# Optimization experiments

Hardware: AMD Instinct MI355X
Metric: run time of the kernel (lower is better)

The kernel has to match this reference:

```python
import jax, jax.numpy as jnp
import numpy as np

V, D, A = 100000, 128, 64
L, N, K = 3, 20000, 16


def setup_inputs() -> dict:
    key = jax.random.key(0)
    k1, k2, k3, k4, k5, k6 = jax.random.split(key, 6)
    Leaf_emb = jax.random.normal(k1, (V, D), dtype=jnp.float32)
    nodes = jax.random.randint(k2, (L, N), 0, V, dtype=jnp.int32)
    neighbors = jax.random.randint(k3, (L, N, K), 0, V, dtype=jnp.int32)
    masks = jnp.zeros((L, N, K), dtype=jnp.float32)  # additive mask, 0 = valid
    weights = jax.random.normal(k4, (L, N, K), dtype=jnp.float32)
    W_att = jax.random.uniform(k5, (2 * D, A), dtype=jnp.float32)
    b_att = jnp.zeros((A,), dtype=jnp.float32)
    v_att = jax.random.uniform(k6, (A,), dtype=jnp.float32)
    return {"Leaf_emb": Leaf_emb, "nodes": nodes, "neighbors": neighbors,
            "masks": masks, "weights": weights,
            "W_att": W_att, "b_att": b_att, "v_att": v_att}


def reference(Leaf_emb, nodes, neighbors, masks, weights, W_att, b_att, v_att):
    # Sequential over L tree levels (fixed, small): each level gathers node and
    # neighbor embeddings, scores neighbors with a 2-layer attention MLP,
    # combines masked-softmax attention with softmax'd structural weights,
    # sums neighbor embeddings and scatters the result back into W_tmp.
    W_tmp = Leaf_emb
    n_levels = nodes.shape[0]
    for i in range(n_levels):
        node = nodes[i]                      # [N] (constant across K in original)
        neighbor = neighbors[i]              # [N, K]
        mask = masks[i]                      # [N, K] additive
        weight = weights[i]                  # [N, K]
        node_tmp = Leaf_emb[node][:, None, :]          # [N, 1, D] from ORIGINAL emb
        neighbor_tmp = W_tmp[neighbor]                 # [N, K, D] from running emb
        node_b = jnp.broadcast_to(node_tmp, neighbor_tmp.shape)
        att_in = jnp.concatenate([node_b, neighbor_tmp], axis=2)  # [N, K, 2D]
        mlp = jax.nn.leaky_relu(att_in @ W_att + b_att, 0.01)     # [N, K, A]
        pre = mlp @ v_att                                         # [N, K]
        att = jax.nn.softmax(pre + mask, axis=1) * jax.nn.softmax(weight, axis=1)
        temp_emb = jnp.einsum('nkd,nk->nd', neighbor_tmp, att)    # [N, D]
        W_tmp = W_tmp.at[node].set(temp_emb)
    return W_tmp
```

## Files before the change

### kernel.cpp

```cpp
#include <hip/hip_runtime.h>
#include <math.h>

#define V 100000
#define D 128
#define A 64
#define LVLS 3
#define NN 20000
#define KK 16
#define BK 32
#define ASTRIDE 34
#define BSTRIDE 68

__global__ __launch_bounds__(256, 2)
void proj_kernel(const float* __restrict__ Wsrc, const float* __restrict__ Wmat,
                 const float* __restrict__ bias, const int* __restrict__ idx,
                 int dst_from_idx, int nrows, float* __restrict__ outp) {
    __shared__ float As[128 * ASTRIDE];
    __shared__ float Bs[BK * BSTRIDE];
    int t = threadIdx.x;
    int tx = t & 15, ty = t >> 4;
    int r0 = blockIdx.x * 128;

    const float* srcp[4];
#pragma unroll
    for (int jj = 0; jj < 4; ++jj) {
        int r = r0 + (t >> 3) + 32 * jj;
        int rr = r < nrows ? r : nrows - 1;
        int s = idx ? idx[rr] : rr;
        srcp[jj] = Wsrc + (size_t)s * D + ((t & 7) << 2);
    }

    float4 bv = make_float4(0.f, 0.f, 0.f, 0.f);
    if (bias) bv = *(const float4*)(bias + 4 * tx);
    float acc[8][4];
#pragma unroll
    for (int i = 0; i < 8; ++i) {
        acc[i][0] = bv.x; acc[i][1] = bv.y; acc[i][2] = bv.z; acc[i][3] = bv.w;
    }

    for (int k0 = 0; k0 < D; k0 += BK) {
#pragma unroll
        for (int jj = 0; jj < 4; ++jj) {
            float4 v = *(const float4*)(srcp[jj] + k0);
            *(float4*)&As[((t >> 3) + 32 * jj) * ASTRIDE + ((t & 7) << 2)] = v;
        }
#pragma unroll
        for (int ss = 0; ss < 2; ++ss) {
            int s = t + 256 * ss;
            int kB = s >> 4, c4 = (s & 15) << 2;
            *(float4*)&Bs[kB * BSTRIDE + c4] =
                *(const float4*)(Wmat + (size_t)(k0 + kB) * A + c4);
        }
        __syncthreads();
#pragma unroll
        for (int kc = 0; kc < BK; kc += 4) {
            float4 b0 = *(const float4*)&Bs[(kc + 0) * BSTRIDE + 4 * tx];
            float4 b1 = *(const float4*)&Bs[(kc + 1) * BSTRIDE + 4 * tx];
            float4 b2 = *(const float4*)&Bs[(kc + 2) * BSTRIDE + 4 * tx];
            float4 b3 = *(const float4*)&Bs[(kc + 3) * BSTRIDE + 4 * tx];
#pragma unroll
            for (int i = 0; i < 8; ++i) {
                float4 a = *(const float4*)&As[(8 * ty + i) * ASTRIDE + kc];
                acc[i][0] = fmaf(a.x, b0.x, acc[i][0]);
                acc[i][0] = fmaf(a.y, b1.x, acc[i][0]);
                acc[i][0] = fmaf(a.z, b2.x, acc[i][0]);
                acc[i][0] = fmaf(a.w, b3.x, acc[i][0]);
                acc[i][1] = fmaf(a.x, b0.y, acc[i][1]);
                acc[i][1] = fmaf(a.y, b1.y, acc[i][1]);
                acc[i][1] = fmaf(a.z, b2.y, acc[i][1]);
                acc[i][1] = fmaf(a.w, b3.y, acc[i][1]);
                acc[i][2] = fmaf(a.x, b0.z, acc[i][2]);
                acc[i][2] = fmaf(a.y, b1.z, acc[i][2]);
                acc[i][2] = fmaf(a.z, b2.z, acc[i][2]);
                acc[i][2] = fmaf(a.w, b3.z, acc[i][2]);
                acc[i][3] = fmaf(a.x, b0.w, acc[i][3]);
                acc[i][3] = fmaf(a.y, b1.w, acc[i][3]);
                acc[i][3] = fmaf(a.z, b2.w, acc[i][3]);
                acc[i][3] = fmaf(a.w, b3.w, acc[i][3]);
            }
        }
        __syncthreads();
    }

#pragma unroll
    for (int i = 0; i < 8; ++i) {
        int gr = r0 + 8 * ty + i;
        if (gr < nrows) {
            int s = idx ? idx[gr] : gr;
            int dst = dst_from_idx ? s : gr;
            float4 o = make_float4(acc[i][0], acc[i][1], acc[i][2], acc[i][3]);
            *(float4*)(outp + (size_t)dst * A + 4 * tx) = o;
        }
    }
}

__global__ __launch_bounds__(256)
void attn_kernel(const float* __restrict__ Wc, const float* __restrict__ proj,
                 const float* __restrict__ nodeproj, const int* __restrict__ neigh,
                 const float* __restrict__ maskp, const float* __restrict__ weightp,
                 const float* __restrict__ v_att, float* __restrict__ tmp) {
    int lane = threadIdx.x & 63;
    int n = blockIdx.x * 4 + (threadIdx.x >> 6);
    int k16 = lane & 15, q = lane >> 4;

    int   nbk = neigh[n * KK + k16];
    float wv  = weightp[n * KK + k16];
    float mk  = maskp[n * KK + k16];

    const float* npr = nodeproj + (size_t)n * A + q * 16;
    const float* var = v_att + q * 16;
    const float* pr  = proj + (size_t)nbk * A + q * 16;

    float part = 0.f;
#pragma unroll
    for (int j = 0; j < 16; j += 4) {
        float4 npv = *(const float4*)(npr + j);
        float4 vav = *(const float4*)(var + j);
        float4 pv  = *(const float4*)(pr + j);
        float x;
        x = npv.x + pv.x; x = fmaxf(x, 0.01f * x); part = fmaf(x, vav.x, part);
        x = npv.y + pv.y; x = fmaxf(x, 0.01f * x); part = fmaf(x, vav.y, part);
        x = npv.z + pv.z; x = fmaxf(x, 0.01f * x); part = fmaf(x, vav.z, part);
        x = npv.w + pv.w; x = fmaxf(x, 0.01f * x); part = fmaf(x, vav.w, part);
    }
    part += __shfl_xor(part, 16);
    part += __shfl_xor(part, 32);
    float pre = part + mk;

    float mp = pre, mw = wv;
#pragma unroll
    for (int off = 8; off >= 1; off >>= 1) {
        mp = fmaxf(mp, __shfl_xor(mp, off));
        mw = fmaxf(mw, __shfl_xor(mw, off));
    }
    float ep = __expf(pre - mp), ew = __expf(wv - mw);
    float sp = ep, sw = ew;
#pragma unroll
    for (int off = 8; off >= 1; off >>= 1) {
        sp += __shfl_xor(sp, off);
        sw += __shfl_xor(sw, off);
    }
    float att = (ep / sp) * (ew / sw);

    float ax = 0.f, ay = 0.f;
#pragma unroll
    for (int k = 0; k < KK; ++k) {
        int nb   = __shfl(nbk, k);
        float ak = __shfl(att, k);
        float2 e = *(const float2*)&Wc[(size_t)nb * D + 2 * lane];
        ax = fmaf(e.x, ak, ax); ay = fmaf(e.y, ak, ay);
    }
    float2 o; o.x = ax; o.y = ay;
    *(float2*)&tmp[(size_t)n * D + 2 * lane] = o;
}

__global__ void amax3_kernel(const int* __restrict__ nodes, int* __restrict__ claims, int total) {
    int i = blockIdx.x * 256 + threadIdx.x;
    if (i < total) {
        int lvl = i / NN, pos = i - lvl * NN;
        atomicMax(&claims[(size_t)lvl * V + nodes[i]], pos);
    }
}

__global__ void scatter_kernel(const int* __restrict__ nodes_l, const int* __restrict__ claim,
                               const float* __restrict__ tmp, float* __restrict__ out, int n) {
    int tid = blockIdx.x * 256 + threadIdx.x;
    int nn = tid >> 7, d = tid & 127;
    if (nn < n) {
        int v = nodes_l[nn];
        if (claim[v] == nn) out[(size_t)v * D + d] = tmp[(size_t)nn * D + d];
    }
}

extern "C" void kernel_launch(void* const* d_in, const int* in_sizes, int n_in,
                              void* d_out, int out_size, void* d_ws, size_t ws_size,
                              hipStream_t stream) {
    const float* Leaf    = (const float*)d_in[0];
    const int*   nodes   = (const int*)d_in[1];
    const int*   neigh   = (const int*)d_in[2];
    const float* masks   = (const float*)d_in[3];
    const float* weights = (const float*)d_in[4];
    const float* Watt    = (const float*)d_in[5];
    const float* batt    = (const float*)d_in[6];
    const float* vatt    = (const float*)d_in[7];
    float* out = (float*)d_out;

    char* ws = (char*)d_ws;
    float* proj     = (float*)ws;
    float* nodeproj = (float*)(ws + (size_t)V * A * 4);
    float* tmp      = (float*)(ws + (size_t)(V * A + LVLS * NN * A) * 4);
    int*   claims   = (int*)(ws + (size_t)(V * A + LVLS * NN * A + NN * D) * 4);

    hipMemcpyAsync(out, Leaf, (size_t)V * D * sizeof(float), hipMemcpyDeviceToDevice, stream);
    hipMemsetAsync(claims, 0xFF, (size_t)LVLS * V * sizeof(int), stream);

    proj_kernel<<<(LVLS * NN + 127) / 128, 256, 0, stream>>>(
        Leaf, Watt, batt, nodes, 0, LVLS * NN, nodeproj);
    proj_kernel<<<(V + 127) / 128, 256, 0, stream>>>(
        out, Watt + D * A, nullptr, nullptr, 0, V, proj);
    amax3_kernel<<<(LVLS * NN + 255) / 256, 256, 0, stream>>>(nodes, claims, LVLS * NN);

    for (int l = 0; l < LVLS; ++l) {
        const int* nodes_l = nodes + l * NN;
        attn_kernel<<<NN / 4, 256, 0, stream>>>(out, proj, nodeproj + (size_t)l * NN * A,
                                                neigh + (size_t)l * NN * KK,
                                                masks + (size_t)l * NN * KK,
                                                weights + (size_t)l * NN * KK, vatt, tmp);
        scatter_kernel<<<(NN * D + 255) / 256, 256, 0, stream>>>(
            nodes_l, claims + (size_t)l * V, tmp, out, NN);
        if (l + 1 < LVLS)
            proj_kernel<<<(NN + 127) / 128, 256, 0, stream>>>(
                out, Watt + D * A, nullptr, nodes_l, 1, NN, proj);
    }
}
```

Measured before the change: 334.5 us.

## Fuse leaf copy into projection, merge scatter with reprojection, widen gather loads

Replaces the separate device copy of Leaf_emb into the output and the two projection launches with one 2D-grid projection kernel. It computes both halves of W_att for all V rows into an interleaved projAll buffer and writes the leaf copy as a side effect. The node-half projection is now indexed by node id instead of being precomputed per level. The per-level scatter and the re-projection kernel are merged into a commit kernel that writes winning rows and their new projections. The attention gather now loads float4 with half-wave splits and a cross-half reduction. This cuts launches and memory passes, at the cost of computing the node projection for all V rows instead of only the 3*N selected ones.

```diff
diff --git a/kernel.cpp b/kernel.cpp
--- a/kernel.cpp
+++ b/kernel.cpp
@@ -10,28 +10,32 @@
 #define BK 32
 #define ASTRIDE 34
 #define BSTRIDE 68
+#define PSTRIDE 128
 
 __global__ __launch_bounds__(256, 2)
-void proj_kernel(const float* __restrict__ Wsrc, const float* __restrict__ Wmat,
-                 const float* __restrict__ bias, const int* __restrict__ idx,
-                 int dst_from_idx, int nrows, float* __restrict__ outp) {
+void projall_kernel(const float* __restrict__ Leaf, const float* __restrict__ Watt,
+                    const float* __restrict__ batt, float* __restrict__ projAll,
+                    float* __restrict__ outp) {
     __shared__ float As[128 * ASTRIDE];
     __shared__ float Bs[BK * BSTRIDE];
     int t = threadIdx.x;
     int tx = t & 15, ty = t >> 4;
     int r0 = blockIdx.x * 128;
+    int half = blockIdx.y;
+    const float* Wmat = Watt + (size_t)half * D * A;
 
     const float* srcp[4];
+    int rg[4];
 #pragma unroll
     for (int jj = 0; jj < 4; ++jj) {
         int r = r0 + (t >> 3) + 32 * jj;
-        int rr = r < nrows ? r : nrows - 1;
-        int s = idx ? idx[rr] : rr;
-        srcp[jj] = Wsrc + (size_t)s * D + ((t & 7) << 2);
+        rg[jj] = r;
+        int rr = r < V ? r : V - 1;
+        srcp[jj] = Leaf + (size_t)rr * D + ((t & 7) << 2);
     }
 
     float4 bv = make_float4(0.f, 0.f, 0.f, 0.f);
-    if (bias) bv = *(const float4*)(bias + 4 * tx);
+    if (half == 0) bv = *(const float4*)(batt + 4 * tx);
     float acc[8][4];
 #pragma unroll
     for (int i = 0; i < 8; ++i) {
@@ -43,6 +47,8 @@
         for (int jj = 0; jj < 4; ++jj) {
             float4 v = *(const float4*)(srcp[jj] + k0);
             *(float4*)&As[((t >> 3) + 32 * jj) * ASTRIDE + ((t & 7) << 2)] = v;
+            if (half == 0 && rg[jj] < V)
+                *(float4*)(outp + (size_t)rg[jj] * D + k0 + ((t & 7) << 2)) = v;
         }
 #pragma unroll
         for (int ss = 0; ss < 2; ++ss) {
@@ -85,31 +91,123 @@
 #pragma unroll
     for (int i = 0; i < 8; ++i) {
         int gr = r0 + 8 * ty + i;
-        if (gr < nrows) {
-            int s = idx ? idx[gr] : gr;
-            int dst = dst_from_idx ? s : gr;
+        if (gr < V) {
             float4 o = make_float4(acc[i][0], acc[i][1], acc[i][2], acc[i][3]);
-            *(float4*)(outp + (size_t)dst * A + 4 * tx) = o;
+            *(float4*)(projAll + (size_t)gr * PSTRIDE + half * 64 + 4 * tx) = o;
+        }
+    }
+}
+
+__global__ __launch_bounds__(256, 2)
+void commit_kernel(const float* __restrict__ tmp, const float* __restrict__ Wmat,
+                   const int* __restrict__ nodes_l, const int* __restrict__ claim,
+                   float* __restrict__ outp, float* __restrict__ projAll, int do_proj) {
+    __shared__ float As[128 * ASTRIDE];
+    __shared__ float Bs[BK * BSTRIDE];
+    int t = threadIdx.x;
+    int tx = t & 15, ty = t >> 4;
+    int r0 = blockIdx.x * 128;
+
+    const float* srcp[4];
+    int vrow[4], win[4];
+#pragma unroll
+    for (int jj = 0; jj < 4; ++jj) {
+        int r = r0 + (t >> 3) + 32 * jj;
+        int rr = r < NN ? r : NN - 1;
+        srcp[jj] = tmp + (size_t)rr * D + ((t & 7) << 2);
+        int v = nodes_l[rr];
+        vrow[jj] = v;
+        win[jj] = (r < NN) && (claim[v] == rr);
+    }
+
+    float acc[8][4];
+#pragma unroll
+    for (int i = 0; i < 8; ++i) {
+        acc[i][0] = 0.f; acc[i][1] = 0.f; acc[i][2] = 0.f; acc[i][3] = 0.f;
+    }
+
+    for (int k0 = 0; k0 < D; k0 += BK) {
+#pragma unroll
+        for (int jj = 0; jj < 4; ++jj) {
+            float4 v = *(const float4*)(srcp[jj] + k0);
+            *(float4*)&As[((t >> 3) + 32 * jj) * ASTRIDE + ((t & 7) << 2)] = v;
+            if (win[jj])
+                *(float4*)(outp + (size_t)vrow[jj] * D + k0 + ((t & 7) << 2)) = v;
+        }
+        if (do_proj) {
+#pragma unroll
+            for (int ss = 0; ss < 2; ++ss) {
+                int s = t + 256 * ss;
+                int kB = s >> 4, c4 = (s & 15) << 2;
+                *(float4*)&Bs[kB * BSTRIDE + c4] =
+                    *(const float4*)(Wmat + (size_t)(k0 + kB) * A + c4);
+            }
+        }
+        __syncthreads();
+        if (do_proj) {
+#pragma unroll
+            for (int kc = 0; kc < BK; kc += 4) {
+                float4 b0 = *(const float4*)&Bs[(kc + 0) * BSTRIDE + 4 * tx];
+                float4 b1 = *(const float4*)&Bs[(kc + 1) * BSTRIDE + 4 * tx];
+                float4 b2 = *(const float4*)&Bs[(kc + 2) * BSTRIDE + 4 * tx];
+                float4 b3 = *(const float4*)&Bs[(kc + 3) * BSTRIDE + 4 * tx];
+#pragma unroll
+                for (int i = 0; i < 8; ++i) {
+                    float4 a = *(const float4*)&As[(8 * ty + i) * ASTRIDE + kc];
+                    acc[i][0] = fmaf(a.x, b0.x, acc[i][0]);
+                    acc[i][0] = fmaf(a.y, b1.x, acc[i][0]);
+                    acc[i][0] = fmaf(a.z, b2.x, acc[i][0]);
+                    acc[i][0] = fmaf(a.w, b3.x, acc[i][0]);
+                    acc[i][1] = fmaf(a.x, b0.y, acc[i][1]);
+                    acc[i][1] = fmaf(a.y, b1.y, acc[i][1]);
+                    acc[i][1] = fmaf(a.z, b2.y, acc[i][1]);
+                    acc[i][1] = fmaf(a.w, b3.y, acc[i][1]);
+                    acc[i][2] = fmaf(a.x, b0.z, acc[i][2]);
+                    acc[i][2] = fmaf(a.y, b1.z, acc[i][2]);
+                    acc[i][2] = fmaf(a.z, b2.z, acc[i][2]);
+                    acc[i][2] = fmaf(a.w, b3.z, acc[i][2]);
+                    acc[i][3] = fmaf(a.x, b0.w, acc[i][3]);
+                    acc[i][3] = fmaf(a.y, b1.w, acc[i][3]);
+                    acc[i][3] = fmaf(a.z, b2.w, acc[i][3]);
+                    acc[i][3] = fmaf(a.w, b3.w, acc[i][3]);
+                }
+            }
+        }
+        __syncthreads();
+    }
+
+    if (do_proj) {
+#pragma unroll
+        for (int i = 0; i < 8; ++i) {
+            int gr = r0 + 8 * ty + i;
+            if (gr < NN) {
+                int v = nodes_l[gr];
+                if (claim[v] == gr) {
+                    float4 o = make_float4(acc[i][0], acc[i][1], acc[i][2], acc[i][3]);
+                    *(float4*)(projAll + (size_t)v * PSTRIDE + 64 + 4 * tx) = o;
+                }
+            }
         }
     }
 }
 
 __global__ __launch_bounds__(256)
-void attn_kernel(const float* __restrict__ Wc, const float* __restrict__ proj,
-                 const float* __restrict__ nodeproj, const int* __restrict__ neigh,
+void attn_kernel(const float* __restrict__ Wc, const float* __restrict__ projAll,
+                 const int* __restrict__ nodes_l, const int* __restrict__ neigh,
                  const float* __restrict__ maskp, const float* __restrict__ weightp,
                  const float* __restrict__ v_att, float* __restrict__ tmp) {
     int lane = threadIdx.x & 63;
     int n = blockIdx.x * 4 + (threadIdx.x >> 6);
     int k16 = lane & 15, q = lane >> 4;
 
+    int   vnode = nodes_l[n];
     int   nbk = neigh[n * KK + k16];
     float wv  = weightp[n * KK + k16];
     float mk  = maskp[n * KK + k16];
 
-    const float* npr = nodeproj + (size_t)n * A + q * 16;
+    const float* npr = projAll + (size_t)vnode * PSTRIDE + q * 16;
     const float* var = v_att + q * 16;
-    const float* pr  = proj + (size_t)nbk * A + q * 16;
+    const float* pr  = projAll + (size_t)nbk * PSTRIDE + 64 + q * 16;
 
     float part = 0.f;
 #pragma unroll
@@ -142,16 +240,23 @@
     }
     float att = (ep / sp) * (ew / sw);
 
-    float ax = 0.f, ay = 0.f;
-#pragma unroll
-    for (int k = 0; k < KK; ++k) {
-        int nb   = __shfl(nbk, k);
-        float ak = __shfl(att, k);
-        float2 e = *(const float2*)&Wc[(size_t)nb * D + 2 * lane];
+    int half = lane >> 5, li = lane & 31;
+    float ax = 0.f, ay = 0.f, az = 0.f, aw = 0.f;
+#pragma unroll
+    for (int m = 0; m < 8; ++m) {
+        int src = 2 * m + half;
+        int nb   = __shfl(nbk, src);
+        float ak = __shfl(att, src);
+        float4 e = *(const float4*)&Wc[(size_t)nb * D + 4 * li];
         ax = fmaf(e.x, ak, ax); ay = fmaf(e.y, ak, ay);
-    }
-    float2 o; o.x = ax; o.y = ay;
-    *(float2*)&tmp[(size_t)n * D + 2 * lane] = o;
+        az = fmaf(e.z, ak, az); aw = fmaf(e.w, ak, aw);
+    }
+    ax += __shfl_xor(ax, 32); ay += __shfl_xor(ay, 32);
+    az += __shfl_xor(az, 32); aw += __shfl_xor(aw, 32);
+    if (half == 0) {
+        float4 o = make_float4(ax, ay, az, aw);
+        *(float4*)&tmp[(size_t)n * D + 4 * li] = o;
+    }
 }
 
 __global__ void amax3_kernel(const int* __restrict__ nodes, int* __restrict__ claims, int total) {
@@ -159,16 +264,6 @@
     if (i < total) {
         int lvl = i / NN, pos = i - lvl * NN;
         atomicMax(&claims[(size_t)lvl * V + nodes[i]], pos);
-    }
-}
-
-__global__ void scatter_kernel(const int* __restrict__ nodes_l, const int* __restrict__ claim,
-                               const float* __restrict__ tmp, float* __restrict__ out, int n) {
-    int tid = blockIdx.x * 256 + threadIdx.x;
-    int nn = tid >> 7, d = tid & 127;
-    if (nn < n) {
-        int v = nodes_l[nn];
-        if (claim[v] == nn) out[(size_t)v * D + d] = tmp[(size_t)nn * D + d];
     }
 }
 
@@ -186,30 +281,23 @@
     float* out = (float*)d_out;
 
     char* ws = (char*)d_ws;
-    float* proj     = (float*)ws;
-    float* nodeproj = (float*)(ws + (size_t)V * A * 4);
-    float* tmp      = (float*)(ws + (size_t)(V * A + LVLS * NN * A) * 4);
-    int*   claims   = (int*)(ws + (size_t)(V * A + LVLS * NN * A + NN * D) * 4);
-
-    hipMemcpyAsync(out, Leaf, (size_t)V * D * sizeof(float), hipMemcpyDeviceToDevice, stream);
+    float* projAll = (float*)ws;
+    float* tmp     = (float*)(ws + (size_t)V * PSTRIDE * 4);
+    int*   claims  = (int*)(ws + (size_t)(V * PSTRIDE + NN * D) * 4);
+
     hipMemsetAsync(claims, 0xFF, (size_t)LVLS * V * sizeof(int), stream);
-
-    proj_kernel<<<(LVLS * NN + 127) / 128, 256, 0, stream>>>(
-        Leaf, Watt, batt, nodes, 0, LVLS * NN, nodeproj);
-    proj_kernel<<<(V + 127) / 128, 256, 0, stream>>>(
-        out, Watt + D * A, nullptr, nullptr, 0, V, proj);
     amax3_kernel<<<(LVLS * NN + 255) / 256, 256, 0, stream>>>(nodes, claims, LVLS * NN);
+    projall_kernel<<<dim3((V + 127) / 128, 2), 256, 0, stream>>>(
+        Leaf, Watt, batt, projAll, out);
 
     for (int l = 0; l < LVLS; ++l) {
         const int* nodes_l = nodes + l * NN;
-        attn_kernel<<<NN / 4, 256, 0, stream>>>(out, proj, nodeproj + (size_t)l * NN * A,
+        attn_kernel<<<NN / 4, 256, 0, stream>>>(out, projAll, nodes_l,
                                                 neigh + (size_t)l * NN * KK,
                                                 masks + (size_t)l * NN * KK,
                                                 weights + (size_t)l * NN * KK, vatt, tmp);
-        scatter_kernel<<<(NN * D + 255) / 256, 256, 0, stream>>>(
-            nodes_l, claims + (size_t)l * V, tmp, out, NN);
-        if (l + 1 < LVLS)
-            proj_kernel<<<(NN + 127) / 128, 256, 0, stream>>>(
-                out, Watt + D * A, nullptr, nodes_l, 1, NN, proj);
-    }
-}
+        commit_kernel<<<(NN + 127) / 128, 256, 0, stream>>>(
+            tmp, Watt + (size_t)D * A, nodes_l, claims + (size_t)l * V, out, projAll,
+            (l + 1 < LVLS) ? 1 : 0);
+    }
+}
```

Measured after the change: 324.6 us. 1.03x faster.
